# Performance work log

Hardware: AMD Instinct MI355X
Metric: run time of the kernel (lower is better)

## Reference

```python
import jax, jax.numpy as jnp
import numpy as np

ANCHORS = np.array([[10.0, 13.0], [16.0, 30.0], [33.0, 23.0]], dtype=np.float32)
IMG_SIZE = 416.0
NUM_CLASSES = 80
IGNORE_THR = 0.5
LAMBDA_XY, LAMBDA_WH, LAMBDA_CONF, LAMBDA_CLS = 1.0, 1.0, 5.0, 1.0
EPS = 1e-12


def setup_inputs() -> dict:
    key = jax.random.key(0)
    k1, k2, k3 = jax.random.split(key, 3)
    bs, A, nc, H, W, T = 32, 3, NUM_CLASSES, 52, 52, 50
    inp = jax.random.normal(k1, (bs, A * (5 + nc), H, W), dtype=jnp.float32)
    cls = jax.random.randint(k2, (bs, T, 1), 0, nc).astype(jnp.float32)
    coords = jax.random.uniform(k3, (bs, T, 4), minval=0.02, maxval=0.98, dtype=jnp.float32)
    targets = jnp.concatenate([cls, coords], axis=-1)  # (class, cx, cy, w, h), normalized
    return {"input": inp, "targets": targets}


def _bce(p, t):
    # elementwise binary cross entropy, sum-reduced by caller; torch convention 0*log(0)=0
    return -(t * jnp.log(jnp.clip(p, EPS, 1.0)) + (1.0 - t) * jnp.log(jnp.clip(1.0 - p, EPS, 1.0)))


def reference(input, targets):
    bs, _, H, W = input.shape
    anchors_px = jnp.asarray(ANCHORS)              # [A,2] in image pixels
    A = anchors_px.shape[0]
    nc = NUM_CLASSES
    stride = IMG_SIZE / H                          # square grid assumed (as in source)
    anchors = anchors_px / stride                  # scaled anchors [A,2]

    pred = input.reshape(bs, A, 5 + nc, H, W).transpose(0, 1, 3, 4, 2)  # [bs,A,H,W,5+nc]
    x = jax.nn.sigmoid(pred[..., 0])
    y = jax.nn.sigmoid(pred[..., 1])
    w = pred[..., 2]
    h = pred[..., 3]
    conf = jax.nn.sigmoid(pred[..., 4])
    pred_cls = jax.nn.sigmoid(pred[..., 5:])

    grid_x = jnp.arange(W, dtype=jnp.float32)[None, None, None, :]
    grid_y = jnp.arange(H, dtype=jnp.float32)[None, None, :, None]
    aw = anchors[:, 0][None, :, None, None]
    ah = anchors[:, 1][None, :, None, None]
    # pred boxes are detached in the original (uses .data)
    px = jax.lax.stop_gradient(x) + grid_x
    py = jax.lax.stop_gradient(y) + grid_y
    pw = jnp.exp(jax.lax.stop_gradient(w)) * aw
    ph = jnp.exp(jax.lax.stop_gradient(h)) * ah

    # ---- vectorized get_target ----
    targets = jax.lax.stop_gradient(targets)
    T = targets.shape[1]
    valid = jnp.sum(targets, axis=-1) > 0          # [bs,T]
    gx = targets[..., 1] * W
    gy = targets[..., 2] * H
    gw = targets[..., 3] * W
    gh = targets[..., 4] * H
    gi = jnp.clip(gx.astype(jnp.int32), 0, W - 1)  # [bs,T]
    gj = jnp.clip(gy.astype(jnp.int32), 0, H - 1)

    # anchor matching: wh-IoU at a common center
    inter_a = jnp.minimum(gw[..., None], anchors[:, 0]) * jnp.minimum(gh[..., None], anchors[:, 1])
    union_a = (gw * gh)[..., None] + anchors[:, 0] * anchors[:, 1] - inter_a
    anch_iou = inter_a / (union_a + 1e-16)         # [bs,T,A]
    best_n = jnp.argmax(anch_iou, axis=-1)         # [bs,T]

    # gt vs all predicted boxes (center-format IoU): [bs,T,A,H,W]
    b1x1 = (gx - gw / 2)[:, :, None, None, None]
    b1x2 = (gx + gw / 2)[:, :, None, None, None]
    b1y1 = (gy - gh / 2)[:, :, None, None, None]
    b1y2 = (gy + gh / 2)[:, :, None, None, None]
    b2x1 = (px - pw / 2)[:, None]
    b2x2 = (px + pw / 2)[:, None]
    b2y1 = (py - ph / 2)[:, None]
    b2y2 = (py + ph / 2)[:, None]
    iw = jnp.clip(jnp.minimum(b1x2, b2x2) - jnp.maximum(b1x1, b2x1), 0.0)
    ih = jnp.clip(jnp.minimum(b1y2, b2y2) - jnp.maximum(b1y1, b2y1), 0.0)
    inter_p = iw * ih
    area1 = (gw * gh)[:, :, None, None, None]
    area2 = (pw * ph)[:, None]
    pred_iou = inter_p / (area1 + area2 - inter_p + 1e-16)  # [bs,T,A,H,W]

    ignore = jnp.any((pred_iou >= IGNORE_THR) & valid[:, :, None, None, None], axis=1)
    noobj_mask = jnp.where(ignore, 0.0, 1.0)       # [bs,A,H,W]

    # scatter targets into the best (anchor, cell) of each gt box; invalid rows dropped
    b_idx = jnp.broadcast_to(jnp.arange(bs)[:, None], (bs, T))
    t_idx = jnp.broadcast_to(jnp.arange(T)[None, :], (bs, T))
    gi_s = jnp.where(valid, gi, W).reshape(-1)     # out-of-range -> mode='drop'
    bf = b_idx.reshape(-1)
    nf = best_n.reshape(-1)
    jf = gj.reshape(-1)

    zeros4 = jnp.zeros((bs, A, H, W), dtype=jnp.float32)
    mask = zeros4.at[bf, nf, jf, gi_s].set(1.0, mode='drop')
    noobj_mask = noobj_mask.at[bf, nf, jf, gi_s].set(0.0, mode='drop')
    tx = zeros4.at[bf, nf, jf, gi_s].set((gx - gi.astype(jnp.float32)).reshape(-1), mode='drop')
    ty = zeros4.at[bf, nf, jf, gi_s].set((gy - gj.astype(jnp.float32)).reshape(-1), mode='drop')
    tw_val = jnp.log(gw / anchors[best_n, 0] + 1e-16)
    th_val = jnp.log(gh / anchors[best_n, 1] + 1e-16)
    tw = zeros4.at[bf, nf, jf, gi_s].set(tw_val.reshape(-1), mode='drop')
    th = zeros4.at[bf, nf, jf, gi_s].set(th_val.reshape(-1), mode='drop')
    tconf_val = pred_iou[b_idx, t_idx, best_n, gj, gi]  # [bs,T] (stored but unused by losses)
    tconf = zeros4.at[bf, nf, jf, gi_s].set(tconf_val.reshape(-1), mode='drop')
    cls_f = jnp.clip(targets[..., 0].astype(jnp.int32), 0, nc - 1).reshape(-1)
    tcls = jnp.zeros((bs, A, H, W, nc), dtype=jnp.float32).at[bf, nf, jf, gi_s, cls_f].set(1.0, mode='drop')

    n_obj = jnp.maximum(jnp.sum(valid.astype(jnp.float32)), 1.0)

    # ---- losses (sum-reduced, as nn.MSELoss/BCELoss(size_average=False)) ----
    loss_x = jnp.sum((x * mask - tx * mask) ** 2) / (2 * n_obj)
    loss_y = jnp.sum((y * mask - ty * mask) ** 2) / (2 * n_obj)
    loss_w = jnp.sum((w * mask - tw * mask) ** 2) / (2 * n_obj)
    loss_h = jnp.sum((h * mask - th * mask) ** 2) / (2 * n_obj)
    # bce(conf*mask, mask): zero where mask==0 (bce(0,0)=0), -log(conf) where mask==1
    loss_conf_obj = -jnp.sum(mask * jnp.log(jnp.clip(conf, EPS, 1.0)))
    # bce(conf*noobj, 0): -log(1-conf) where noobj==1, zero elsewhere
    loss_conf_noobj = -jnp.sum(noobj_mask * jnp.log(jnp.clip(1.0 - conf, EPS, 1.0)))
    loss_conf = loss_conf_obj / n_obj + 0.2 * loss_conf_noobj / n_obj
    loss_cls = jnp.sum(mask[..., None] * _bce(pred_cls, tcls)) / n_obj

    loss = (loss_x * LAMBDA_XY + loss_y * LAMBDA_XY + loss_w * LAMBDA_WH + loss_h * LAMBDA_WH
            + loss_conf * LAMBDA_CONF + loss_cls * LAMBDA_CLS)

    # global_step < 12800 branch (early anchor-prior loss), always applied here
    a_loss = (jnp.sum((x - 0.5) ** 2) + jnp.sum((y - 0.5) ** 2)
              + jnp.sum(w ** 2) + jnp.sum(h ** 2)) / (2 * n_obj)
    loss = loss + 0.1 * a_loss
    return loss
```

## Files before the change

### kernel.cpp

```cpp
#include <hip/hip_runtime.h>
#include <math.h>

#define BS 32
#define NA 3
#define NC 80
#define HH 52
#define WW 52
#define TPER 50
#define NTT (BS * TPER)
#define HW (HH * WW)
#define CPB (NA * HW)
#define CH (5 + NC)
#define CELLS_PER_BLK 1024
#define CBPB 8
#define NCELLBLK (BS * CBPB)
#define OBJ_PAIRS 25
#define NOBJBLK (BS * OBJ_PAIRS)
#define NBLK (NCELLBLK + NOBJBLK)

__device__ __forceinline__ float fexp(float x) { return __builtin_amdgcn_exp2f(x * 1.4426950408889634f); }
__device__ __forceinline__ float flog(float x) { return __builtin_amdgcn_logf(x) * 0.6931471805599453f; }
__device__ __forceinline__ float sigm(float v) { return __builtin_amdgcn_rcpf(1.0f + fexp(-v)); }

__device__ __forceinline__ float wave_red(float t) {
    #pragma unroll
    for (int off = 32; off > 0; off >>= 1) t += __shfl_down(t, off);
    return t;
}


__global__ __launch_bounds__(256) void k_main(const float* __restrict__ in,
                                              const float* __restrict__ tgt,
                                              float2* __restrict__ ws)
{
    __shared__ float4 sbox[TPER];
    __shared__ int scell[TPER], scls[TPER];
    __shared__ unsigned sbm[CELLS_PER_BLK / 32];
    __shared__ float wred[4];
    const int tid = threadIdx.x;
    const float aw[3] = {1.25f, 2.0f, 4.125f};
    const float ah[3] = {1.625f, 3.75f, 2.875f};
    const float raw[3] = {0.8f, 0.5f, 0.24242424242424243f};
    const float rah[3] = {0.6153846153846154f, 0.26666666666666666f, 0.34782608695652173f};

    float term = 0.0f;
    float flag = 0.0f;

    if (blockIdx.x < NCELLBLK) {
        const int b  = blockIdx.x >> 3;
        const int lo = (blockIdx.x & 7) * CELLS_PER_BLK;
        if (tid < CELLS_PER_BLK / 32) sbm[tid] = 0u;
        int mycell = -1;
        if (tid < TPER) {
            const float* p = tgt + (size_t)(b * TPER + tid) * 5;
            float c0 = p[0], c1 = p[1], c2 = p[2], c3 = p[3], c4 = p[4];
            bool valid = (c0 + c1 + c2 + c3 + c4) > 0.0f;
            float gx = c1 * WW, gy = c2 * HH, gw = c3 * WW, gh = c4 * HH;
            int gi = (int)gx; gi = gi < 0 ? 0 : (gi > WW - 1 ? WW - 1 : gi);
            int gj = (int)gy; gj = gj < 0 ? 0 : (gj > HH - 1 ? HH - 1 : gj);
            int bn = 0;
            {
                float bi = fminf(gw, aw[0]) * fminf(gh, ah[0]);
                float bu = gw * gh + aw[0] * ah[0] - bi;
                #pragma unroll
                for (int a = 1; a < 3; ++a) {
                    float ia = fminf(gw, aw[a]) * fminf(gh, ah[a]);
                    float ua = gw * gh + aw[a] * ah[a] - ia;
                    if (ia * bu > bi * ua) { bn = a; bi = ia; bu = ua; }
                }
            }
            if (valid) {
                sbox[tid] = make_float4(gx - 0.5f * gw, gx + 0.5f * gw,
                                        gy - 0.5f * gh, gy + 0.5f * gh);
                mycell = bn * HW + gj * WW + gi;
            } else {
                sbox[tid] = make_float4(1e30f, 1e30f, 1e30f, 1e30f);
            }
        }
        __syncthreads();
        if (mycell >= lo && mycell < lo + CELLS_PER_BLK)
            atomicOr(&sbm[(mycell - lo) >> 5], 1u << ((mycell - lo) & 31));
        __syncthreads();

        const int idx0 = lo + tid;
        float P1[4], P2[4], Q1[4], Q2[4], A2[4], CF[4];
        bool ACT[4], IGN[4] = {false, false, false, false};
        #pragma unroll
        for (int k = 0; k < 4; ++k) {
            int idx = idx0 + k * 256;
            ACT[k] = idx < CPB;
            P1[k] = 0.0f; P2[k] = 0.0f; Q1[k] = 0.0f; Q2[k] = 0.0f;
            A2[k] = 1e30f; CF[k] = 0.5f;
            if (ACT[k]) {
                int a = idx / HW;
                int r = idx - a * HW;
                int yy = r / WW;
                int xx = r - yy * WW;
                const float* base = in + ((size_t)b * (NA * CH) + a * CH) * HW + r;
                float xr = base[0], yr = base[HW], wr = base[2 * HW],
                      hr = base[3 * HW], cr = base[4 * HW];
                float sx = sigm(xr), sy = sigm(yr);
                CF[k] = sigm(cr);
                float px = sx + (float)xx, py = sy + (float)yy;
                float pw = fexp(wr) * aw[a], ph = fexp(hr) * ah[a];
                P1[k] = px - 0.5f * pw; P2[k] = px + 0.5f * pw;
                Q1[k] = py - 0.5f * ph; Q2[k] = py + 0.5f * ph;
                A2[k] = pw * ph + 1e-16f;
                term += 0.05f * ((sx - 0.5f) * (sx - 0.5f) + (sy - 0.5f) * (sy - 0.5f)
                                 + wr * wr + hr * hr);
            }
        }
        #pragma unroll 2
        for (int t = 0; t < TPER; ++t) {
            float4 bx = sbox[t];
            float ar = (bx.y - bx.x) * (bx.w - bx.z);
            #pragma unroll
            for (int k = 0; k < 4; ++k) {
                float iw = fmaxf(fminf(bx.y, P2[k]) - fmaxf(bx.x, P1[k]), 0.0f);
                float ih = fmaxf(fminf(bx.w, Q2[k]) - fmaxf(bx.z, Q1[k]), 0.0f);
                float inter = iw * ih;
                IGN[k] = IGN[k] || (3.0f * inter >= ar + A2[k]);
            }
        }
        #pragma unroll
        for (int k = 0; k < 4; ++k) {
            int d = tid + k * 256;
            bool ist = (sbm[d >> 5] >> (d & 31)) & 1u;
            if (ACT[k] && !IGN[k] && !ist)
                term += -flog(fmaxf(1.0f - CF[k], 1e-12f));
        }
    } else {
        const int o = blockIdx.x - NCELLBLK;
        const int b = o / OBJ_PAIRS;
        const int pair = o - b * OBJ_PAIRS;
        const int tA = 2 * pair;
        if (tid < TPER) {
            const float* p = tgt + (size_t)(b * TPER + tid) * 5;
            float c0 = p[0], c1 = p[1], c2 = p[2], c3 = p[3], c4 = p[4];
            bool valid = (c0 + c1 + c2 + c3 + c4) > 0.0f;
            float gx = c1 * WW, gy = c2 * HH, gw = c3 * WW, gh = c4 * HH;
            int gi = (int)gx; gi = gi < 0 ? 0 : (gi > WW - 1 ? WW - 1 : gi);
            int gj = (int)gy; gj = gj < 0 ? 0 : (gj > HH - 1 ? HH - 1 : gj);
            int bn = 0;
            {
                float bi = fminf(gw, aw[0]) * fminf(gh, ah[0]);
                float bu = gw * gh + aw[0] * ah[0] - bi;
                #pragma unroll
                for (int a = 1; a < 3; ++a) {
                    float ia = fminf(gw, aw[a]) * fminf(gh, ah[a]);
                    float ua = gw * gh + aw[a] * ah[a] - ia;
                    if (ia * bu > bi * ua) { bn = a; bi = ia; bu = ua; }
                }
            }
            scell[tid] = valid ? (bn * HW + gj * WW + gi) : -1;
            int cls = (int)c0; cls = cls < 0 ? 0 : (cls > NC - 1 ? NC - 1 : cls);
            scls[tid] = cls;
        }
        __syncthreads();
        const int half = tid >> 7;
        const int myT = tA + half;
        const int k = tid & 127;
        const int cell = scell[myT];
        int a = 0, r = 0;
        float v = 0.0f;
        if (cell >= 0 && k < 85) {
            a = cell / HW;
            r = cell - a * HW;
            v = in[((size_t)b * (NA * CH) + a * CH + k) * HW + r];
        }
        const int lane = tid & 63;
        bool m = (lane < TPER) && (cell >= 0) && (scell[lane] == cell);
        unsigned long long mask = __ballot(m);
        bool owner = (cell >= 0) && ((mask >> (myT + 1)) == 0ULL);
        if (owner) {
            if (k < 5) {
                const float* p = tgt + (size_t)(b * TPER + myT) * 5;
                if (k == 0) {
                    float gx = p[1] * WW; int gi = r - (r / WW) * WW;
                    float d = sigm(v) - (gx - (float)gi); term = 0.5f * d * d;
                } else if (k == 1) {
                    float gy = p[2] * HH; int gj = r / WW;
                    float d = sigm(v) - (gy - (float)gj); term = 0.5f * d * d;
                } else if (k == 2) {
                    float d = v - flog(p[3] * WW * raw[a] + 1e-16f); term = 0.5f * d * d;
                } else if (k == 3) {
                    float d = v - flog(p[4] * HH * rah[a] + 1e-16f); term = 0.5f * d * d;
                } else {
                    term = -5.0f * flog(fmaxf(sigm(v), 1e-12f));
                }
            } else if (k < 85) {
                int c = k - 5;
                bool pos = false;
                unsigned long long mm = mask;
                while (mm) { int t2 = __ffsll(mm) - 1; mm &= mm - 1; pos = pos || (scls[t2] == c); }
                float p = sigm(v);
                term = pos ? -flog(fmaxf(p, 1e-12f)) : -flog(fmaxf(1.0f - p, 1e-12f));
            }
        }
        if (tid == 0)
            flag = (scell[tA] >= 0 ? 1.0f : 0.0f) + (scell[tA + 1] >= 0 ? 1.0f : 0.0f);
    }

    float tr = wave_red(term);
    if ((tid & 63) == 0) wred[tid >> 6] = tr;
    __syncthreads();
    if (tid == 0)
        ws[blockIdx.x] = make_float2(wred[0] + wred[1] + wred[2] + wred[3], flag);
}

__global__ __launch_bounds__(256) void k_final(const float2* __restrict__ ws,
                                               float* __restrict__ out)
{
    const int tid = threadIdx.x;
    const float4* w4 = (const float4*)ws;
    float s = 0.0f, nv = 0.0f;
    for (int i = tid; i < NBLK / 2; i += 256) {
        float4 v = w4[i];
        s += v.x + v.z;
        nv += v.y + v.w;
    }
    __shared__ float wr0[4], wr1[4];
    s = wave_red(s);
    nv = wave_red(nv);
    if ((tid & 63) == 0) { wr0[tid >> 6] = s; wr1[tid >> 6] = nv; }
    __syncthreads();
    if (tid == 0) {
        float S = wr0[0] + wr0[1] + wr0[2] + wr0[3];
        float N = wr1[0] + wr1[1] + wr1[2] + wr1[3];
        out[0] = S / fmaxf(N, 1.0f);
    }
}

extern "C" void kernel_launch(void* const* d_in, const int* in_sizes, int n_in,
                              void* d_out, int out_size, void* d_ws, size_t ws_size,
                              hipStream_t stream)
{
    const float* in = (const float*)d_in[0];
    const float* tgt = (const float*)d_in[1];
    float2* ws = (float2*)d_ws;

    k_main<<<NBLK, 256, 0, stream>>>(in, tgt, ws);
    k_final<<<1, 256, 0, stream>>>(ws, (float*)d_out);
}
```

Measured before the change: 18.53 us.

## Vectorize per-cell loads with float4 and replace shared target tables with wave shuffles

Each thread in the cell blocks now handles four consecutive cells, so the five prediction channels come in as float4 loads. The index and anchor math is done once per thread rather than per cell, and the layout keeps each group of four inside one row and one anchor plane. The object blocks now compute target cells and classes in every wave and share them with __shfl and __ballot, which removes the shared arrays and a __syncthreads. The costs are some repeated target decoding in each wave and a different access pattern for the conflict-bitmap reads.

Measured after the change: 17.50 us. -5.6%, faster.

```diff
diff --git a/kernel.cpp b/kernel.cpp
--- a/kernel.cpp
+++ b/kernel.cpp
@@ -34,7 +34,6 @@
                                               float2* __restrict__ ws)
 {
     __shared__ float4 sbox[TPER];
-    __shared__ int scell[TPER], scls[TPER];
     __shared__ unsigned sbm[CELLS_PER_BLK / 32];
     __shared__ float wred[4];
     const int tid = threadIdx.x;
@@ -82,32 +81,39 @@
             atomicOr(&sbm[(mycell - lo) >> 5], 1u << ((mycell - lo) & 31));
         __syncthreads();
 
-        const int idx0 = lo + tid;
+        const int q0 = lo + 4 * tid;
+        const bool actq = q0 < CPB;
         float P1[4], P2[4], Q1[4], Q2[4], A2[4], CF[4];
-        bool ACT[4], IGN[4] = {false, false, false, false};
+        bool IGN[4] = {false, false, false, false};
         #pragma unroll
-        for (int k = 0; k < 4; ++k) {
-            int idx = idx0 + k * 256;
-            ACT[k] = idx < CPB;
-            P1[k] = 0.0f; P2[k] = 0.0f; Q1[k] = 0.0f; Q2[k] = 0.0f;
-            A2[k] = 1e30f; CF[k] = 0.5f;
-            if (ACT[k]) {
-                int a = idx / HW;
-                int r = idx - a * HW;
-                int yy = r / WW;
-                int xx = r - yy * WW;
-                const float* base = in + ((size_t)b * (NA * CH) + a * CH) * HW + r;
-                float xr = base[0], yr = base[HW], wr = base[2 * HW],
-                      hr = base[3 * HW], cr = base[4 * HW];
-                float sx = sigm(xr), sy = sigm(yr);
-                CF[k] = sigm(cr);
-                float px = sx + (float)xx, py = sy + (float)yy;
-                float pw = fexp(wr) * aw[a], ph = fexp(hr) * ah[a];
+        for (int k = 0; k < 4; ++k) { P1[k]=0; P2[k]=0; Q1[k]=0; Q2[k]=0; A2[k]=1e30f; CF[k]=0.5f; }
+        if (actq) {
+            const int a  = q0 / HW;
+            const int r  = q0 - a * HW;
+            const int yy = r / WW;
+            const int xx0 = r - yy * WW;
+            const float* plane = in + ((size_t)b * (NA * CH) + a * CH) * HW + r;
+            float4 X = *(const float4*)(plane);
+            float4 Y = *(const float4*)(plane + HW);
+            float4 Wv = *(const float4*)(plane + 2 * HW);
+            float4 Hv = *(const float4*)(plane + 3 * HW);
+            float4 Cv = *(const float4*)(plane + 4 * HW);
+            float xs[4] = {X.x, X.y, X.z, X.w};
+            float ys[4] = {Y.x, Y.y, Y.z, Y.w};
+            float zs[4] = {Wv.x, Wv.y, Wv.z, Wv.w};
+            float hs[4] = {Hv.x, Hv.y, Hv.z, Hv.w};
+            float cs[4] = {Cv.x, Cv.y, Cv.z, Cv.w};
+            #pragma unroll
+            for (int k = 0; k < 4; ++k) {
+                float sx = sigm(xs[k]), sy = sigm(ys[k]);
+                CF[k] = sigm(cs[k]);
+                float px = sx + (float)(xx0 + k), py = sy + (float)yy;
+                float pw = fexp(zs[k]) * aw[a], ph = fexp(hs[k]) * ah[a];
                 P1[k] = px - 0.5f * pw; P2[k] = px + 0.5f * pw;
                 Q1[k] = py - 0.5f * ph; Q2[k] = py + 0.5f * ph;
                 A2[k] = pw * ph + 1e-16f;
                 term += 0.05f * ((sx - 0.5f) * (sx - 0.5f) + (sy - 0.5f) * (sy - 0.5f)
-                                 + wr * wr + hr * hr);
+                                 + zs[k] * zs[k] + hs[k] * hs[k]);
             }
         }
         #pragma unroll 2
@@ -122,20 +128,28 @@
                 IGN[k] = IGN[k] || (3.0f * inter >= ar + A2[k]);
             }
         }
-        #pragma unroll
-        for (int k = 0; k < 4; ++k) {
-            int d = tid + k * 256;
-            bool ist = (sbm[d >> 5] >> (d & 31)) & 1u;
-            if (ACT[k] && !IGN[k] && !ist)
-                term += -flog(fmaxf(1.0f - CF[k], 1e-12f));
+        if (actq) {
+            #pragma unroll
+            for (int k = 0; k < 4; ++k) {
+                int d = 4 * tid + k;
+                bool ist = (sbm[d >> 5] >> (d & 31)) & 1u;
+                if (!IGN[k] && !ist)
+                    term += -flog(fmaxf(1.0f - CF[k], 1e-12f));
+            }
         }
     } else {
         const int o = blockIdx.x - NCELLBLK;
         const int b = o / OBJ_PAIRS;
         const int pair = o - b * OBJ_PAIRS;
         const int tA = 2 * pair;
-        if (tid < TPER) {
-            const float* p = tgt + (size_t)(b * TPER + tid) * 5;
+        const int lane = tid & 63;
+        const int wid = tid >> 6;
+        const int myT = tA + (wid >> 1);
+        const int k = ((wid & 1) << 6) | lane;
+
+        int celll = -1, clsl = 0;
+        if (lane < TPER) {
+            const float* p = tgt + (size_t)(b * TPER + lane) * 5;
             float c0 = p[0], c1 = p[1], c2 = p[2], c3 = p[3], c4 = p[4];
             bool valid = (c0 + c1 + c2 + c3 + c4) > 0.0f;
             float gx = c1 * WW, gy = c2 * HH, gw = c3 * WW, gh = c4 * HH;
@@ -152,15 +166,14 @@
                     if (ia * bu > bi * ua) { bn = a; bi = ia; bu = ua; }
                 }
             }
-            scell[tid] = valid ? (bn * HW + gj * WW + gi) : -1;
+            celll = valid ? (bn * HW + gj * WW + gi) : -1;
             int cls = (int)c0; cls = cls < 0 ? 0 : (cls > NC - 1 ? NC - 1 : cls);
-            scls[tid] = cls;
-        }
-        __syncthreads();
-        const int half = tid >> 7;
-        const int myT = tA + half;
-        const int k = tid & 127;
-        const int cell = scell[myT];
+            clsl = cls;
+        }
+        const int cell = __shfl(celll, myT);
+        bool mt = (lane < TPER) && (cell >= 0) && (celll == cell);
+        unsigned long long mask = __ballot(mt);
+        bool owner = (cell >= 0) && ((mask >> (myT + 1)) == 0ULL);
         int a = 0, r = 0;
         float v = 0.0f;
         if (cell >= 0 && k < 85) {
@@ -168,11 +181,7 @@
             r = cell - a * HW;
             v = in[((size_t)b * (NA * CH) + a * CH + k) * HW + r];
         }
-        const int lane = tid & 63;
-        bool m = (lane < TPER) && (cell >= 0) && (scell[lane] == cell);
-        unsigned long long mask = __ballot(m);
-        bool owner = (cell >= 0) && ((mask >> (myT + 1)) == 0ULL);
-        if (owner) {
+        if (owner && k < 85) {
             if (k < 5) {
                 const float* p = tgt + (size_t)(b * TPER + myT) * 5;
                 if (k == 0) {
@@ -188,17 +197,20 @@
                 } else {
                     term = -5.0f * flog(fmaxf(sigm(v), 1e-12f));
                 }
-            } else if (k < 85) {
+            } else {
                 int c = k - 5;
                 bool pos = false;
                 unsigned long long mm = mask;
-                while (mm) { int t2 = __ffsll(mm) - 1; mm &= mm - 1; pos = pos || (scls[t2] == c); }
+                while (mm) {
+                    int t2 = __ffsll(mm) - 1; mm &= mm - 1;
+                    pos = pos || (__shfl(clsl, t2) == c);
+                }
                 float p = sigm(v);
                 term = pos ? -flog(fmaxf(p, 1e-12f)) : -flog(fmaxf(1.0f - p, 1e-12f));
             }
         }
-        if (tid == 0)
-            flag = (scell[tA] >= 0 ? 1.0f : 0.0f) + (scell[tA + 1] >= 0 ? 1.0f : 0.0f);
+        int cA = __shfl(celll, tA), cB = __shfl(celll, tA + 1);
+        flag = (cA >= 0 ? 1.0f : 0.0f) + (cB >= 0 ? 1.0f : 0.0f);
     }
 
     float tr = wave_red(term);
```
